# Optimization experiments

Hardware: AMD Instinct MI355X
Metric: run time of the kernel (lower is better)

Reference implementation:

```python
import jax, jax.numpy as jnp
import numpy as np

N = 8192
H_CHANNELS = 2048
HEADS = 16
D = H_CHANNELS // HEADS  # 128


def setup_inputs() -> dict:
    key = jax.random.key(0)
    k1, k2, k3 = jax.random.split(key, 3)
    x0 = jax.random.normal(k1, (N, H_CHANNELS), dtype=jnp.float32)
    # boolean mask: True entries are masked out (set to -inf)
    mask = jax.random.randint(k2, (N, N), 0, 2).astype(jnp.bool_)
    # torch Linear weight layout: [out_features, in_features] = [3*d, h_channels]
    W_qkv = jax.random.normal(k3, (3 * D, H_CHANNELS), dtype=jnp.float32) * (1.0 / np.sqrt(H_CHANNELS))
    return {"x0": x0, "mask": mask, "W_qkv": W_qkv}


def reference(x0, mask, W_qkv):
    # qkv = x0 @ W^T : [N, 3d]
    qkv = x0 @ W_qkv.T
    q, k, v = jnp.split(qkv, 3, axis=-1)          # each [N, d]
    att_logits = (q @ k.T) / D                    # [N, N]  (note: scale is /d, not /sqrt(d))
    att_logits = jnp.where(mask, -jnp.inf, att_logits)
    att = jax.nn.softmax(att_logits, axis=-1)     # [N, N]
    # dropout p=0.0 (eval mode) -> identity
    return att @ v                                # [N, d]
```

## Files before the change

kernel.cpp:

```cpp
#include <hip/hip_runtime.h>
#include <hip/hip_bf16.h>

typedef __attribute__((ext_vector_type(8))) short short8;
typedef __attribute__((ext_vector_type(4))) float f32x4;

#define NTOK 8192
#define HCH  2048
#define DDIM 128

__device__ __forceinline__ unsigned short f2bf(float f) {
    __hip_bfloat16 h = __float2bfloat16(f);
    return *reinterpret_cast<unsigned short*>(&h);
}

__global__ void detect_kernel(const unsigned int* __restrict__ X,
                              const unsigned int* __restrict__ M,
                              int* __restrict__ flags)
{
    const int lane = threadIdx.x & 63;
    unsigned int e = (X[lane] >> 7) & 0xFF;
    unsigned long long hb = __ballot(e >= 110 && e <= 140);

    bool w_ok = true, h_ok = true, b_ok = true;
#pragma unroll
    for (int i = 0; i < 16; i++) {
        unsigned int u = M[lane + 64 * i];
        if (!(u == 0u || u == 1u || u == 0x3F800000u)) w_ok = false;
        unsigned int h0 = u & 0xFFFFu, h1 = u >> 16;
        bool o0 = (h0 == 0u || h0 == 0x3F80u || h0 == 0x3C00u || h0 == 1u);
        bool o1 = (h1 == 0u || h1 == 0x3F80u || h1 == 0x3C00u || h1 == 1u);
        if (!(o0 && o1)) h_ok = false;
        unsigned int b0 = u & 0xFF, b1 = (u >> 8) & 0xFF,
                     b2 = (u >> 16) & 0xFF, b3 = u >> 24;
        if (b0 > 1u || b1 > 1u || b2 > 1u || b3 > 1u) b_ok = false;
    }
    bool allw = __all(w_ok), allh = __all(h_ok), allb = __all(b_ok);
    if (lane == 0) {
        flags[0] = (__popcll(hb) < 32) ? 1 : 0;
        flags[1] = allw ? 0 : (allb ? 1 : (allh ? 2 : 3));
    }
}

__global__ __launch_bounds__(256) void conv_w(
    const void* __restrict__ Wv, const int* __restrict__ flags,
    unsigned short* __restrict__ Wbf)
{
    int t = blockIdx.x * 256 + threadIdx.x;
    size_t off = (size_t)t * 8;
    if (flags[0] != 0) {
        const float* Wf = (const float*)Wv;
        float4 a = *reinterpret_cast<const float4*>(Wf + off);
        float4 b = *reinterpret_cast<const float4*>(Wf + off + 4);
        unsigned short o[8] = { f2bf(a.x), f2bf(a.y), f2bf(a.z), f2bf(a.w),
                                f2bf(b.x), f2bf(b.y), f2bf(b.z), f2bf(b.w) };
        *reinterpret_cast<uint4*>(Wbf + off) = *reinterpret_cast<uint4*>(o);
    } else {
        *reinterpret_cast<uint4*>(Wbf + off) =
            *reinterpret_cast<const uint4*>((const unsigned short*)Wv + off);
    }
}

__global__ __launch_bounds__(256) void mask_pack(
    const void* __restrict__ maskv, const int* __restrict__ flags,
    unsigned char* __restrict__ Mp)
{
    const int mmode = flags[1];
    const int NB = NTOK * (NTOK / 8);
    int t0 = blockIdx.x * 256 + threadIdx.x;
    for (int b = t0; b < NB; b += 2048 * 256) {
        unsigned int byte = 0;
        if (mmode == 0) {
            const uint4* p = reinterpret_cast<const uint4*>(
                (const unsigned int*)maskv + (size_t)b * 8);
            uint4 a = p[0], c = p[1];
            byte = (a.x != 0u) | ((a.y != 0u) << 1) | ((a.z != 0u) << 2) | ((a.w != 0u) << 3)
                 | ((c.x != 0u) << 4) | ((c.y != 0u) << 5) | ((c.z != 0u) << 6) | ((c.w != 0u) << 7);
        } else if (mmode == 1) {
            unsigned long long v = *reinterpret_cast<const unsigned long long*>(
                (const unsigned char*)maskv + (size_t)b * 8);
#pragma unroll
            for (int k = 0; k < 8; k++)
                byte |= (((v >> (8 * k)) & 0xFFull) != 0ull) << k;
        } else if (mmode == 2) {
            uint4 a = *reinterpret_cast<const uint4*>(
                (const unsigned short*)maskv + (size_t)b * 8);
            byte = ((a.x & 0xFFFFu) != 0u) | ((a.x >> 16 != 0u) << 1)
                 | (((a.y & 0xFFFFu) != 0u) << 2) | ((a.y >> 16 != 0u) << 3)
                 | (((a.z & 0xFFFFu) != 0u) << 4) | ((a.z >> 16 != 0u) << 5)
                 | (((a.w & 0xFFFFu) != 0u) << 6) | ((a.w >> 16 != 0u) << 7);
        } else {
            byte = ((const unsigned char*)maskv)[b];
        }
        Mp[b] = (unsigned char)byte;
    }
}

__global__ __launch_bounds__(256) void qkv_gemm(
    const void* __restrict__ Xv, const unsigned short* __restrict__ Wbf,
    const int* __restrict__ flags,
    unsigned short* __restrict__ Qb, unsigned short* __restrict__ Kb,
    unsigned short* __restrict__ Vb)
{
    __shared__ unsigned short Wsm[128 * 64];
    __shared__ unsigned short Xsm[32 * 64];
    const int tid  = threadIdx.x;
    const int lane = tid & 63, w = tid >> 6;
    const int c = lane & 15, g = lane >> 4;
    const int q0 = blockIdx.x * 32;
    const int n0 = blockIdx.y * 128;
    const bool f32in = (flags[0] != 0);
    const float*          Xf = (const float*)Xv;
    const unsigned short* Xb = (const unsigned short*)Xv;

    f32x4 acc[4];
#pragma unroll
    for (int i = 0; i < 4; i++) acc[i] = (f32x4){0.f, 0.f, 0.f, 0.f};

    const int xrow = tid >> 3, xc8 = tid & 7;
    const int arow = (w & 1) * 16 + c;

    for (int kk = 0; kk < HCH; kk += 64) {
        __syncthreads();
#pragma unroll
        for (int i = 0; i < 4; i++) {
            int cid = tid + 256 * i;
            int n = cid >> 3, c8 = cid & 7;
            uint4 v = *reinterpret_cast<const uint4*>(Wbf + (size_t)(n0 + n) * HCH + kk + c8 * 8);
            *reinterpret_cast<uint4*>(&Wsm[(n * 8 + (c8 ^ (n & 7))) * 8]) = v;
        }
        {
            unsigned short o[8];
            if (f32in) {
                const float* p = Xf + (size_t)(q0 + xrow) * HCH + kk + xc8 * 8;
                float4 a = *reinterpret_cast<const float4*>(p);
                float4 b = *reinterpret_cast<const float4*>(p + 4);
                o[0]=f2bf(a.x); o[1]=f2bf(a.y); o[2]=f2bf(a.z); o[3]=f2bf(a.w);
                o[4]=f2bf(b.x); o[5]=f2bf(b.y); o[6]=f2bf(b.z); o[7]=f2bf(b.w);
            } else {
                *reinterpret_cast<uint4*>(o) =
                    *reinterpret_cast<const uint4*>(Xb + (size_t)(q0 + xrow) * HCH + kk + xc8 * 8);
            }
            *reinterpret_cast<uint4*>(&Xsm[(xrow * 8 + (xc8 ^ (xrow & 7))) * 8]) =
                *reinterpret_cast<uint4*>(o);
        }
        __syncthreads();
#pragma unroll
        for (int ks = 0; ks < 2; ks++) {
            short8 af = *reinterpret_cast<const short8*>(
                &Xsm[(arow * 8 + ((ks * 4 + g) ^ (c & 7))) * 8]);
#pragma unroll
            for (int nt = 0; nt < 4; nt++) {
                int n = (w >> 1) * 64 + nt * 16 + c;
                short8 bf = *reinterpret_cast<const short8*>(
                    &Wsm[(n * 8 + ((ks * 4 + g) ^ (c & 7))) * 8]);
                acc[nt] = __builtin_amdgcn_mfma_f32_16x16x32_bf16(af, bf, acc[nt], 0, 0, 0);
            }
        }
    }
    unsigned short* dst = (blockIdx.y == 0) ? Qb : (blockIdx.y == 1) ? Kb : Vb;
#pragma unroll
    for (int nt = 0; nt < 4; nt++) {
        int n = (w >> 1) * 64 + nt * 16 + c;
#pragma unroll
        for (int r = 0; r < 4; r++) {
            int rr = q0 + (w & 1) * 16 + g * 4 + r;
            dst[(size_t)rr * DDIM + n] = f2bf(acc[nt][r]);
        }
    }
}

__global__ __launch_bounds__(256) void vtrans(
    const unsigned short* __restrict__ V, unsigned short* __restrict__ VT)
{
    __shared__ unsigned short T[32 * 33];
    const int t = threadIdx.x;
    const int k0 = blockIdx.x * 32, d0 = blockIdx.y * 32;
    {
        int key = t >> 3, dq = (t & 7) * 4;
        ushort4 v = *reinterpret_cast<const ushort4*>(V + (size_t)(k0 + key) * DDIM + d0 + dq);
        T[(dq + 0) * 33 + key] = v.x;
        T[(dq + 1) * 33 + key] = v.y;
        T[(dq + 2) * 33 + key] = v.z;
        T[(dq + 3) * 33 + key] = v.w;
    }
    __syncthreads();
    {
        int d = t >> 3, kq = (t & 7) * 4;
        ushort4 o;
        o.x = T[d * 33 + kq + 0]; o.y = T[d * 33 + kq + 1];
        o.z = T[d * 33 + kq + 2]; o.w = T[d * 33 + kq + 3];
        *reinterpret_cast<ushort4*>(VT + (size_t)(d0 + d) * NTOK + k0 + kq) = o;
    }
}

__global__ __launch_bounds__(256, 4) void attn_part(
    const unsigned short* __restrict__ Qb, const unsigned short* __restrict__ Kb,
    const unsigned short* __restrict__ VT, const unsigned long long* __restrict__ Mp,
    _Float16* __restrict__ Opart, float* __restrict__ lpart, int kps)
{
    __shared__ unsigned short Ksm[64 * 128];
    __shared__ unsigned short Vsm[128 * 64];
    __shared__ unsigned short Psm[4 * 16 * 64];
    const int tid  = threadIdx.x;
    const int lane = tid & 63, w = tid >> 6;
    const int c = lane & 15, g = lane >> 4;
    const int q0 = blockIdx.y * 64;
    const int split = blockIdx.x;
    const int kbase = split * kps;
    const int niter = kps >> 6;
    const int tb0 = kbase >> 6;
    unsigned short* Pw = &Psm[w * 16 * 64];

    short8 qf[4];
#pragma unroll
    for (int ks = 0; ks < 4; ks++)
        qf[ks] = *reinterpret_cast<const short8*>(Qb + (size_t)(q0 + w * 16 + c) * DDIM + ks * 32 + g * 8);

    short8 ones;
#pragma unroll
    for (int i = 0; i < 8; i++) ones[i] = (short)0x3F80;

    f32x4 accO[8];
#pragma unroll
    for (int i = 0; i < 8; i++) accO[i] = (f32x4){0.f, 0.f, 0.f, 0.f};
    f32x4 accL = (f32x4){0.f, 0.f, 0.f, 0.f};

    unsigned long long mp[4], mpn[4];
#pragma unroll
    for (int r = 0; r < 4; r++)
        mp[r] = Mp[(size_t)(q0 + w * 16 + g * 4 + r) * 128 + tb0];

    for (int t = 0; t < niter; t++) {
        const int k0 = kbase + t * 64;
        __syncthreads();
#pragma unroll
        for (int i = 0; i < 4; i++) {
            int cid = tid + 256 * i;
            int rowk = cid >> 4, c16 = cid & 15;
            uint4 v = *reinterpret_cast<const uint4*>(Kb + (size_t)(k0 + rowk) * DDIM + c16 * 8);
            *reinterpret_cast<uint4*>(&Ksm[(rowk * 16 + (c16 ^ (rowk & 15))) * 8]) = v;
        }
#pragma unroll
        for (int i = 0; i < 4; i++) {
            int cid = tid + 256 * i;
            int d = cid >> 3, c8 = cid & 7;
            uint4 v = *reinterpret_cast<const uint4*>(VT + (size_t)d * NTOK + k0 + c8 * 8);
            *reinterpret_cast<uint4*>(&Vsm[(d * 8 + (c8 ^ (d & 7))) * 8]) = v;
        }
        if (t + 1 < niter) {
#pragma unroll
            for (int r = 0; r < 4; r++)
                mpn[r] = Mp[(size_t)(q0 + w * 16 + g * 4 + r) * 128 + tb0 + t + 1];
        }
        __syncthreads();

        f32x4 sacc[4];
#pragma unroll
        for (int nt = 0; nt < 4; nt++) {
            sacc[nt] = (f32x4){0.f, 0.f, 0.f, 0.f};
#pragma unroll
            for (int ks = 0; ks < 4; ks++) {
                short8 bf = *reinterpret_cast<const short8*>(
                    &Ksm[((nt * 16 + c) * 16 + ((ks * 4 + g) ^ c)) * 8]);
                sacc[nt] = __builtin_amdgcn_mfma_f32_16x16x32_bf16(qf[ks], bf, sacc[nt], 0, 0, 0);
            }
        }

#pragma unroll
        for (int nt = 0; nt < 4; nt++)
#pragma unroll
            for (int r = 0; r < 4; r++) {
                bool mv = (mp[r] >> (nt * 16 + c)) & 1ull;
                float p = mv ? 0.f : __expf(sacc[nt][r] * (1.0f / 128.0f));
                int row = g * 4 + r;
                Pw[(row * 8 + ((nt * 2 + (c >> 3)) ^ (row & 7))) * 8 + (c & 7)] = f2bf(p);
            }
#pragma unroll
        for (int r = 0; r < 4; r++) mp[r] = mpn[r];

#pragma unroll
        for (int ks2 = 0; ks2 < 2; ks2++) {
            short8 af = *reinterpret_cast<const short8*>(
                &Pw[(c * 8 + ((ks2 * 4 + g) ^ (c & 7))) * 8]);
            accL = __builtin_amdgcn_mfma_f32_16x16x32_bf16(af, ones, accL, 0, 0, 0);
#pragma unroll
            for (int dt = 0; dt < 8; dt++) {
                short8 bfv = *reinterpret_cast<const short8*>(
                    &Vsm[((dt * 16 + c) * 8 + ((ks2 * 4 + g) ^ (c & 7))) * 8]);
                accO[dt] = __builtin_amdgcn_mfma_f32_16x16x32_bf16(af, bfv, accO[dt], 0, 0, 0);
            }
        }
    }

    _Float16* Op = Opart + (size_t)split * NTOK * DDIM;
#pragma unroll
    for (int nt = 0; nt < 8; nt++)
#pragma unroll
        for (int r = 0; r < 4; r++)
            Op[(size_t)(q0 + w * 16 + g * 4 + r) * DDIM + nt * 16 + c] = (_Float16)accO[nt][r];
    if (c == 0) {
#pragma unroll
        for (int r = 0; r < 4; r++)
            lpart[(size_t)split * NTOK + q0 + w * 16 + g * 4 + r] = accL[r];
    }
}

__global__ __launch_bounds__(256) void combine(
    const _Float16* __restrict__ Opart, const float* __restrict__ lpart,
    float* __restrict__ out, int nsplit)
{
    int idx = blockIdx.x * 256 + threadIdx.x;
    int row = idx >> 7;
    const size_t S = (size_t)NTOK * DDIM;
    float den = 0.f, num = 0.f;
    for (int s = 0; s < nsplit; s++) {
        den += lpart[(size_t)s * NTOK + row];
        num += (float)Opart[(size_t)s * S + idx];
    }
    out[idx] = (den > 0.f) ? (num / den) : 0.f;
}

extern "C" void kernel_launch(void* const* d_in, const int* in_sizes, int n_in,
                              void* d_out, int out_size, void* d_ws, size_t ws_size,
                              hipStream_t stream)
{
    const void* X = d_in[0]; const void* mask = d_in[1]; const void* W = d_in[2];
    {
        const void* x_ = nullptr; const void* m_ = nullptr; const void* w_ = nullptr;
        for (int i = 0; i < n_in; i++) {
            if (in_sizes[i] == 16777216) x_ = d_in[i];
            else if (in_sizes[i] == 67108864) m_ = d_in[i];
            else if (in_sizes[i] == 786432) w_ = d_in[i];
        }
        if (x_ && m_ && w_) { X = x_; mask = m_; W = w_; }
    }
    float* out = (float*)d_out;

    const int nsplit = (ws_size >= (33ull << 20)) ? 8 : 4;
    const int kps = NTOK / nsplit;

    char* ws = (char*)d_ws;
    unsigned short* Qb  = (unsigned short*)(ws);
    unsigned short* Kb  = (unsigned short*)(ws + (2ull << 20));
    unsigned short* VT  = (unsigned short*)(ws + (4ull << 20));
    unsigned long long* Mpk = (unsigned long long*)(ws + (6ull << 20));
    _Float16*       Opart = (_Float16*)(ws + (14ull << 20));
    unsigned short* Wbf = (unsigned short*)(ws + (14ull << 20));
    unsigned short* Vb  = (unsigned short*)(ws + (14ull << 20) + (1536ull << 10));
    float*          lpart = (float*)(ws + (14ull << 20) + ((size_t)nsplit << 21));
    int*            flags = (int*)((char*)lpart + (128ull << 10));

    detect_kernel<<<1, 64, 0, stream>>>((const unsigned int*)X, (const unsigned int*)mask, flags);
    conv_w<<<dim3(384), 256, 0, stream>>>(W, flags, Wbf);
    mask_pack<<<dim3(2048), 256, 0, stream>>>(mask, flags, (unsigned char*)Mpk);
    qkv_gemm<<<dim3(256, 3), 256, 0, stream>>>(X, Wbf, flags, Qb, Kb, Vb);
    vtrans<<<dim3(256, 4), 256, 0, stream>>>(Vb, VT);
    attn_part<<<dim3(nsplit, 128), 256, 0, stream>>>(Qb, Kb, VT, Mpk, Opart, lpart, kps);
    combine<<<dim3(4096), 256, 0, stream>>>(Opart, lpart, out, nsplit);
}
```

Measured before the change: 616.5 us.

## Process two 16-row query tiles per wave to reuse K/V tiles

Each wave now handles 32 query rows (two 16-row tiles) instead of 16, so every K/V tile staged in shared memory feeds twice as many MFMAs. The number of query blocks is halved, the split count is fixed at 8, and partial outputs are written as packed 16-byte vectors in a custom layout that the combine kernel decodes. The cost is roughly double the accumulator registers with the occupancy hint removed, which may reduce waves per CU. The fixed split also assumes the workspace is large enough.

```diff
diff --git a/kernel.cpp b/kernel.cpp
--- a/kernel.cpp
+++ b/kernel.cpp
@@ -7,9 +7,16 @@
 #define NTOK 8192
 #define HCH  2048
 #define DDIM 128
+#define NSPLIT 8
+#define KPS   (NTOK / NSPLIT)
+#define NITER (KPS / 64)
 
 __device__ __forceinline__ unsigned short f2bf(float f) {
     __hip_bfloat16 h = __float2bfloat16(f);
+    return *reinterpret_cast<unsigned short*>(&h);
+}
+__device__ __forceinline__ unsigned short f2h(float f) {
+    _Float16 h = (_Float16)f;
     return *reinterpret_cast<unsigned short*>(&h);
 }
 
@@ -193,10 +200,10 @@
     }
 }
 
-__global__ __launch_bounds__(256, 4) void attn_part(
+__global__ __launch_bounds__(256) void attn_part(
     const unsigned short* __restrict__ Qb, const unsigned short* __restrict__ Kb,
     const unsigned short* __restrict__ VT, const unsigned long long* __restrict__ Mp,
-    _Float16* __restrict__ Opart, float* __restrict__ lpart, int kps)
+    _Float16* __restrict__ Opart, float* __restrict__ lpart)
 {
     __shared__ unsigned short Ksm[64 * 128];
     __shared__ unsigned short Vsm[128 * 64];
@@ -204,33 +211,40 @@
     const int tid  = threadIdx.x;
     const int lane = tid & 63, w = tid >> 6;
     const int c = lane & 15, g = lane >> 4;
-    const int q0 = blockIdx.y * 64;
     const int split = blockIdx.x;
-    const int kbase = split * kps;
-    const int niter = kps >> 6;
+    const int qb    = blockIdx.y;
+    const int q0 = qb * 128;
+    const int kbase = split * KPS;
     const int tb0 = kbase >> 6;
     unsigned short* Pw = &Psm[w * 16 * 64];
 
-    short8 qf[4];
-#pragma unroll
-    for (int ks = 0; ks < 4; ks++)
-        qf[ks] = *reinterpret_cast<const short8*>(Qb + (size_t)(q0 + w * 16 + c) * DDIM + ks * 32 + g * 8);
+    short8 qf[2][4];
+#pragma unroll
+    for (int rt = 0; rt < 2; rt++)
+#pragma unroll
+        for (int ks = 0; ks < 4; ks++)
+            qf[rt][ks] = *reinterpret_cast<const short8*>(
+                Qb + (size_t)(q0 + w * 32 + rt * 16 + c) * DDIM + ks * 32 + g * 8);
 
     short8 ones;
 #pragma unroll
     for (int i = 0; i < 8; i++) ones[i] = (short)0x3F80;
 
-    f32x4 accO[8];
-#pragma unroll
-    for (int i = 0; i < 8; i++) accO[i] = (f32x4){0.f, 0.f, 0.f, 0.f};
-    f32x4 accL = (f32x4){0.f, 0.f, 0.f, 0.f};
-
-    unsigned long long mp[4], mpn[4];
-#pragma unroll
-    for (int r = 0; r < 4; r++)
-        mp[r] = Mp[(size_t)(q0 + w * 16 + g * 4 + r) * 128 + tb0];
-
-    for (int t = 0; t < niter; t++) {
+    f32x4 accO[2][8];
+#pragma unroll
+    for (int rt = 0; rt < 2; rt++)
+#pragma unroll
+        for (int i = 0; i < 8; i++) accO[rt][i] = (f32x4){0.f, 0.f, 0.f, 0.f};
+    f32x4 accL[2] = {(f32x4){0.f,0.f,0.f,0.f}, (f32x4){0.f,0.f,0.f,0.f}};
+
+    unsigned long long mp[2][4], mpn[2][4];
+#pragma unroll
+    for (int rt = 0; rt < 2; rt++)
+#pragma unroll
+        for (int r = 0; r < 4; r++)
+            mp[rt][r] = Mp[(size_t)(q0 + w * 32 + rt * 16 + g * 4 + r) * 128 + tb0];
+
+    for (int t = 0; t < NITER; t++) {
         const int k0 = kbase + t * 64;
         __syncthreads();
 #pragma unroll
@@ -247,75 +261,93 @@
             uint4 v = *reinterpret_cast<const uint4*>(VT + (size_t)d * NTOK + k0 + c8 * 8);
             *reinterpret_cast<uint4*>(&Vsm[(d * 8 + (c8 ^ (d & 7))) * 8]) = v;
         }
-        if (t + 1 < niter) {
+        if (t + 1 < NITER) {
+#pragma unroll
+            for (int rt = 0; rt < 2; rt++)
+#pragma unroll
+                for (int r = 0; r < 4; r++)
+                    mpn[rt][r] = Mp[(size_t)(q0 + w * 32 + rt * 16 + g * 4 + r) * 128 + tb0 + t + 1];
+        }
+        __syncthreads();
+
+#pragma unroll
+        for (int rt = 0; rt < 2; rt++) {
+            f32x4 sacc[4];
+#pragma unroll
+            for (int nt = 0; nt < 4; nt++) {
+                sacc[nt] = (f32x4){0.f, 0.f, 0.f, 0.f};
+#pragma unroll
+                for (int ks = 0; ks < 4; ks++) {
+                    short8 bf = *reinterpret_cast<const short8*>(
+                        &Ksm[((nt * 16 + c) * 16 + ((ks * 4 + g) ^ c)) * 8]);
+                    sacc[nt] = __builtin_amdgcn_mfma_f32_16x16x32_bf16(qf[rt][ks], bf, sacc[nt], 0, 0, 0);
+                }
+            }
+#pragma unroll
+            for (int nt = 0; nt < 4; nt++)
+#pragma unroll
+                for (int r = 0; r < 4; r++) {
+                    bool mv = (mp[rt][r] >> (nt * 16 + c)) & 1ull;
+                    float p = mv ? 0.f : __expf(sacc[nt][r] * (1.0f / 128.0f));
+                    int row = g * 4 + r;
+                    Pw[(row * 8 + ((nt * 2 + (c >> 3)) ^ (row & 7))) * 8 + (c & 7)] = f2bf(p);
+                }
+#pragma unroll
+            for (int ks2 = 0; ks2 < 2; ks2++) {
+                short8 af = *reinterpret_cast<const short8*>(
+                    &Pw[(c * 8 + ((ks2 * 4 + g) ^ (c & 7))) * 8]);
+                accL[rt] = __builtin_amdgcn_mfma_f32_16x16x32_bf16(af, ones, accL[rt], 0, 0, 0);
+#pragma unroll
+                for (int dt = 0; dt < 8; dt++) {
+                    short8 bfv = *reinterpret_cast<const short8*>(
+                        &Vsm[((dt * 16 + c) * 8 + ((ks2 * 4 + g) ^ (c & 7))) * 8]);
+                    accO[rt][dt] = __builtin_amdgcn_mfma_f32_16x16x32_bf16(af, bfv, accO[rt][dt], 0, 0, 0);
+                }
+            }
+        }
+#pragma unroll
+        for (int rt = 0; rt < 2; rt++)
+#pragma unroll
+            for (int r = 0; r < 4; r++) mp[rt][r] = mpn[rt][r];
+    }
+
+    _Float16* Ob = Opart + ((size_t)split * 64 + qb) * (128 * DDIM) + (size_t)w * 4096;
+#pragma unroll
+    for (int rt = 0; rt < 2; rt++)
+#pragma unroll
+        for (int r = 0; r < 4; r++) {
+            unsigned short o[8];
+#pragma unroll
+            for (int dt = 0; dt < 8; dt++) o[dt] = f2h(accO[rt][dt][r]);
+            *reinterpret_cast<uint4*>(Ob + ((((rt * 4 + r) * 4 + g) * 16 + c) * 8)) =
+                *reinterpret_cast<uint4*>(o);
+        }
+    if (c == 0) {
+#pragma unroll
+        for (int rt = 0; rt < 2; rt++)
 #pragma unroll
             for (int r = 0; r < 4; r++)
-                mpn[r] = Mp[(size_t)(q0 + w * 16 + g * 4 + r) * 128 + tb0 + t + 1];
-        }
-        __syncthreads();
-
-        f32x4 sacc[4];
-#pragma unroll
-        for (int nt = 0; nt < 4; nt++) {
-            sacc[nt] = (f32x4){0.f, 0.f, 0.f, 0.f};
-#pragma unroll
-            for (int ks = 0; ks < 4; ks++) {
-                short8 bf = *reinterpret_cast<const short8*>(
-                    &Ksm[((nt * 16 + c) * 16 + ((ks * 4 + g) ^ c)) * 8]);
-                sacc[nt] = __builtin_amdgcn_mfma_f32_16x16x32_bf16(qf[ks], bf, sacc[nt], 0, 0, 0);
-            }
-        }
-
-#pragma unroll
-        for (int nt = 0; nt < 4; nt++)
-#pragma unroll
-            for (int r = 0; r < 4; r++) {
-                bool mv = (mp[r] >> (nt * 16 + c)) & 1ull;
-                float p = mv ? 0.f : __expf(sacc[nt][r] * (1.0f / 128.0f));
-                int row = g * 4 + r;
-                Pw[(row * 8 + ((nt * 2 + (c >> 3)) ^ (row & 7))) * 8 + (c & 7)] = f2bf(p);
-            }
-#pragma unroll
-        for (int r = 0; r < 4; r++) mp[r] = mpn[r];
-
-#pragma unroll
-        for (int ks2 = 0; ks2 < 2; ks2++) {
-            short8 af = *reinterpret_cast<const short8*>(
-                &Pw[(c * 8 + ((ks2 * 4 + g) ^ (c & 7))) * 8]);
-            accL = __builtin_amdgcn_mfma_f32_16x16x32_bf16(af, ones, accL, 0, 0, 0);
-#pragma unroll
-            for (int dt = 0; dt < 8; dt++) {
-                short8 bfv = *reinterpret_cast<const short8*>(
-                    &Vsm[((dt * 16 + c) * 8 + ((ks2 * 4 + g) ^ (c & 7))) * 8]);
-                accO[dt] = __builtin_amdgcn_mfma_f32_16x16x32_bf16(af, bfv, accO[dt], 0, 0, 0);
-            }
-        }
-    }
-
-    _Float16* Op = Opart + (size_t)split * NTOK * DDIM;
-#pragma unroll
-    for (int nt = 0; nt < 8; nt++)
-#pragma unroll
-        for (int r = 0; r < 4; r++)
-            Op[(size_t)(q0 + w * 16 + g * 4 + r) * DDIM + nt * 16 + c] = (_Float16)accO[nt][r];
-    if (c == 0) {
-#pragma unroll
-        for (int r = 0; r < 4; r++)
-            lpart[(size_t)split * NTOK + q0 + w * 16 + g * 4 + r] = accL[r];
+                lpart[(size_t)split * NTOK + q0 + w * 32 + rt * 16 + g * 4 + r] = accL[rt][r];
     }
 }
 
 __global__ __launch_bounds__(256) void combine(
     const _Float16* __restrict__ Opart, const float* __restrict__ lpart,
-    float* __restrict__ out, int nsplit)
+    float* __restrict__ out)
 {
     int idx = blockIdx.x * 256 + threadIdx.x;
-    int row = idx >> 7;
+    int row = idx >> 7, d = idx & 127;
+    int qb = row >> 7, win = row & 127;
+    int w = win >> 5, rt = (win >> 4) & 1, g = (win >> 2) & 3, r = win & 3;
+    int nt = d >> 4, c = d & 15;
+    size_t off = (size_t)qb * (128 * DDIM) + (size_t)w * 4096
+               + ((((rt * 4 + r) * 4 + g) * 16 + c) * 8) + nt;
     const size_t S = (size_t)NTOK * DDIM;
     float den = 0.f, num = 0.f;
-    for (int s = 0; s < nsplit; s++) {
+#pragma unroll
+    for (int s = 0; s < NSPLIT; s++) {
         den += lpart[(size_t)s * NTOK + row];
-        num += (float)Opart[(size_t)s * S + idx];
+        num += (float)Opart[(size_t)s * S + off];
     }
     out[idx] = (den > 0.f) ? (num / den) : 0.f;
 }
@@ -335,9 +367,6 @@
         if (x_ && m_ && w_) { X = x_; mask = m_; W = w_; }
     }
     float* out = (float*)d_out;
-
-    const int nsplit = (ws_size >= (33ull << 20)) ? 8 : 4;
-    const int kps = NTOK / nsplit;
 
     char* ws = (char*)d_ws;
     unsigned short* Qb  = (unsigned short*)(ws);
@@ -347,14 +376,14 @@
     _Float16*       Opart = (_Float16*)(ws + (14ull << 20));
     unsigned short* Wbf = (unsigned short*)(ws + (14ull << 20));
     unsigned short* Vb  = (unsigned short*)(ws + (14ull << 20) + (1536ull << 10));
-    float*          lpart = (float*)(ws + (14ull << 20) + ((size_t)nsplit << 21));
-    int*            flags = (int*)((char*)lpart + (128ull << 10));
+    float*          lpart = (float*)(ws + (30ull << 20));
+    int*            flags = (int*)(ws + (30ull << 20) + (512ull << 10));
 
     detect_kernel<<<1, 64, 0, stream>>>((const unsigned int*)X, (const unsigned int*)mask, flags);
     conv_w<<<dim3(384), 256, 0, stream>>>(W, flags, Wbf);
     mask_pack<<<dim3(2048), 256, 0, stream>>>(mask, flags, (unsigned char*)Mpk);
     qkv_gemm<<<dim3(256, 3), 256, 0, stream>>>(X, Wbf, flags, Qb, Kb, Vb);
     vtrans<<<dim3(256, 4), 256, 0, stream>>>(Vb, VT);
-    attn_part<<<dim3(nsplit, 128), 256, 0, stream>>>(Qb, Kb, VT, Mpk, Opart, lpart, kps);
-    combine<<<dim3(4096), 256, 0, stream>>>(Opart, lpart, out, nsplit);
-}
+    attn_part<<<dim3(NSPLIT, 64), 256, 0, stream>>>(Qb, Kb, VT, Mpk, Opart, lpart);
+    combine<<<dim3(4096), 256, 0, stream>>>(Opart, lpart, out);
+}
```

After: 544.7 us. 1.13x faster.
